# Kernel optimization log

Measured on AMD Instinct MI355X. Metric: run time of the kernel, lower is better.

The kernel has to match this reference:

```python
import jax, jax.numpy as jnp
import numpy as np

N_NODES = 50000
N_EDGES = 800000
IN_DIM = 100
HID = 128
OUT = 128
EPS = 1e-5


def setup_inputs() -> dict:
    key = jax.random.key(0)
    ks = jax.random.split(key, 12)
    x = jax.random.normal(ks[0], (N_NODES, IN_DIM), dtype=jnp.float32)
    edge_index = jax.random.randint(ks[1], (2, N_EDGES), 0, N_NODES, dtype=jnp.int32)
    def lin(k, i, o):
        return jax.random.normal(k, (i, o), dtype=jnp.float32) * (1.0 / np.sqrt(i))
    return {
        "x": x,
        "edge_index": edge_index,
        "W_l0": lin(ks[2], IN_DIM, HID),  # neighbor transform, layer 0
        "b_l0": jnp.zeros((HID,), jnp.float32),
        "W_r0": lin(ks[3], IN_DIM, HID),  # root transform, layer 0
        "gamma0": jnp.ones((HID,), jnp.float32),
        "beta0": jnp.zeros((HID,), jnp.float32),
        "W_l1": lin(ks[4], HID, OUT),
        "b_l1": jnp.zeros((OUT,), jnp.float32),
        "W_r1": lin(ks[5], HID, OUT),
        "gamma1": jnp.ones((OUT,), jnp.float32),
        "beta1": jnp.zeros((OUT,), jnp.float32),
    }


def _sage_conv(x, edge_index, W_l, b_l, W_r):
    # PyG SAGEConv (mean aggr): out = lin_l(mean_{j->i} x_j) + lin_r(x_i)
    src, dst = edge_index[0], edge_index[1]
    n = x.shape[0]
    msg_sum = jax.ops.segment_sum(x[src], dst, num_segments=n)        # [N, d_in]
    cnt = jax.ops.segment_sum(jnp.ones((src.shape[0],), x.dtype), dst, num_segments=n)
    agg = msg_sum / jnp.maximum(cnt, 1.0)[:, None]
    return agg @ W_l + b_l + x @ W_r


def _batch_norm(x, gamma, beta):
    # BatchNorm1d with batch statistics (training-mode math, biased var)
    mean = x.mean(axis=0)
    var = x.var(axis=0)
    return gamma * (x - mean) / jnp.sqrt(var + EPS) + beta


def reference(x, edge_index, W_l0, b_l0, W_r0, gamma0, beta0, W_l1, b_l1, W_r1, gamma1, beta1):
    # Layer 0: SAGEConv -> BN -> ReLU (dropout off for determinism)
    h = _sage_conv(x, edge_index, W_l0, b_l0, W_r0)
    h = jax.nn.relu(_batch_norm(h, gamma0, beta0))
    # Layer 1 (last): SAGEConv -> BN
    h = _sage_conv(h, edge_index, W_l1, b_l1, W_r1)
    return _batch_norm(h, gamma1, beta1)
```

## Files before the change

### kernel.cpp

```cpp
#include <hip/hip_runtime.h>
#include <hip/hip_bf16.h>

#define N_NODES 50000
#define N_EDGES 800000
#define NPAD    50048
#define IN_DIM  100
#define HID     128
#define BN_EPS  1e-5f

#define BSHIFT  6
#define BUCKS   782
#define BSTRIDE 2048
#define BCAP    2048
#define NSLICE  16

typedef unsigned int uint;
typedef unsigned short u16;
typedef __attribute__((ext_vector_type(8))) unsigned short us8;
typedef __attribute__((ext_vector_type(8))) short s8;
typedef __attribute__((ext_vector_type(4))) float f4;

__device__ __forceinline__ u16 f2bf(float f) {
    uint u = __builtin_bit_cast(uint, f);
    uint r = (u + 0x7FFFu + ((u >> 16) & 1u)) >> 16;
    return (u16)r;
}
__device__ __forceinline__ uint pack2(float a, float b) {
    return (uint)f2bf(a) | ((uint)f2bf(b) << 16);
}
__device__ __forceinline__ float bflo(uint p) { return __builtin_bit_cast(float, p << 16); }
__device__ __forceinline__ float bfhi(uint p) { return __builtin_bit_cast(float, p & 0xFFFF0000u); }

__global__ void init_cursor(int* __restrict__ bcursor) {
    int b = blockIdx.x * 256 + threadIdx.x;
    if (b < BUCKS) bcursor[b] = b * BSTRIDE;
}

__global__ __launch_bounds__(1024) void bucket_scatter_blk(
    const int* __restrict__ src, const int* __restrict__ dst,
    int* __restrict__ bcursor, uint* __restrict__ ebuf) {
    __shared__ int h[BUCKS];
    __shared__ int gb[BUCKS];
    int t = threadIdx.x;
    for (int i = t; i < BUCKS; i += 1024) h[i] = 0;
    __syncthreads();
    int base = blockIdx.x * 8192;
    int myb[8]; uint myv[8];
    #pragma unroll
    for (int r = 0; r < 8; ++r) {
        int e = base + r * 1024 + t;
        int b = -1; uint val = 0;
        if (e < N_EDGES) {
            int d = dst[e];
            b = d >> BSHIFT;
            val = (uint)src[e] | ((uint)(d & 63) << 16);
            atomicAdd(&h[b], 1);
        }
        myb[r] = b; myv[r] = val;
    }
    __syncthreads();
    for (int i = t; i < BUCKS; i += 1024) {
        int c = h[i];
        gb[i] = c ? atomicAdd(&bcursor[i], c) : 0;
        h[i] = 0;
    }
    __syncthreads();
    #pragma unroll
    for (int r = 0; r < 8; ++r) {
        int b = myb[r];
        if (b >= 0) {
            int pos = gb[b] + atomicAdd(&h[b], 1);
            ebuf[pos] = myv[r];
        }
    }
}

__global__ void cast_x_kernel(const float* __restrict__ x, u16* __restrict__ xb) {
    int idx = blockIdx.x * blockDim.x + threadIdx.x;
    if (idx >= NPAD * 128) return;
    int row = idx >> 7, k = idx & 127;
    float v = (row < N_NODES && k < IN_DIM) ? x[row * IN_DIM + k] : 0.f;
    xb[idx] = f2bf(v);
}

__global__ void cast_w_kernel(const float* __restrict__ W_l0, const float* __restrict__ W_r0,
                              const float* __restrict__ W_l1, const float* __restrict__ W_r1,
                              u16* __restrict__ d) {
    int w = blockIdx.y;
    const float* s = (w == 0) ? W_l0 : (w == 1) ? W_r0 : (w == 2) ? W_l1 : W_r1;
    int Ks = (w < 2) ? IN_DIM : HID;
    int idx = blockIdx.x * 256 + threadIdx.x;
    int n = idx >> 7, k = idx & 127;
    float v = (k < Ks) ? s[k * 128 + n] : 0.f;
    d[w * 16384 + idx] = f2bf(v);
}

__global__ __launch_bounds__(512) void agg_gemm(
    const uint* __restrict__ ebuf, const int* __restrict__ bcursor,
    const u16* __restrict__ X,
    const u16* __restrict__ WtL, const u16* __restrict__ WtR,
    const float* __restrict__ bias, float* __restrict__ out,
    float* __restrict__ gstats) {
    __shared__ u16 Aagg[64][136];
    __shared__ uint eL[BCAP];
    __shared__ u16 srcL[BCAP];
    __shared__ int cnt[64], ro[65], cur[64];
    __shared__ float s1L[128], s2L[128];

    int b = blockIdx.x;
    int t = threadIdx.x;
    int row0 = b * 64;
    int wave = t >> 6, lane = t & 63;
    int quad = lane >> 4, sub = lane & 15, l16 = lane & 15;

    int n = bcursor[b] - b * BSTRIDE;
    if (n > BCAP) n = BCAP;
    if (t < 64) cnt[t] = 0;
    if (t < 128) { s1L[t] = 0.f; s2L[t] = 0.f; }
    __syncthreads();
    for (int i = t; i < n; i += 512) {
        uint p = ebuf[b * BSTRIDE + i];
        eL[i] = p;
        atomicAdd(&cnt[p >> 16], 1);
    }
    __syncthreads();
    if (t < 64) {
        int v = cnt[t];
        int s = v;
        #pragma unroll
        for (int off = 1; off < 64; off <<= 1) {
            int u = __shfl_up(s, off, 64);
            if (t >= off) s += u;
        }
        ro[t] = s - v;
        cur[t] = s - v;
        if (t == 63) ro[64] = s;
    }
    __syncthreads();
    for (int i = t; i < n; i += 512) {
        uint p = eL[i];
        int pos = atomicAdd(&cur[p >> 16], 1);
        srcL[pos] = (u16)(p & 0xFFFFu);
    }
    __syncthreads();

    #pragma unroll
    for (int ni = 0; ni < 8; ++ni) {
        int nl = wave * 8 + ni;
        int node = row0 + nl;
        if (node >= N_NODES) {
            if (quad == 0) {
                uint4 z = make_uint4(0, 0, 0, 0);
                *(uint4*)&Aagg[nl][sub * 8] = z;
            }
            continue;
        }
        int rb = ro[nl], re = ro[nl + 1];
        float a0 = 0.f, a1 = 0.f, a2 = 0.f, a3 = 0.f;
        float a4 = 0.f, a5 = 0.f, a6 = 0.f, a7 = 0.f;
        int e = rb;
        for (; e + 16 <= re; e += 16) {
            int s0 = srcL[e + quad];
            int s1 = srcL[e + 4 + quad];
            int s2 = srcL[e + 8 + quad];
            int s3 = srcL[e + 12 + quad];
            uint4 v0 = ((const uint4*)(X + (size_t)s0 * 128))[sub];
            uint4 v1 = ((const uint4*)(X + (size_t)s1 * 128))[sub];
            uint4 v2 = ((const uint4*)(X + (size_t)s2 * 128))[sub];
            uint4 v3 = ((const uint4*)(X + (size_t)s3 * 128))[sub];
            a0 += (bflo(v0.x) + bflo(v1.x)) + (bflo(v2.x) + bflo(v3.x));
            a1 += (bfhi(v0.x) + bfhi(v1.x)) + (bfhi(v2.x) + bfhi(v3.x));
            a2 += (bflo(v0.y) + bflo(v1.y)) + (bflo(v2.y) + bflo(v3.y));
            a3 += (bfhi(v0.y) + bfhi(v1.y)) + (bfhi(v2.y) + bfhi(v3.y));
            a4 += (bflo(v0.z) + bflo(v1.z)) + (bflo(v2.z) + bflo(v3.z));
            a5 += (bfhi(v0.z) + bfhi(v1.z)) + (bfhi(v2.z) + bfhi(v3.z));
            a6 += (bflo(v0.w) + bflo(v1.w)) + (bflo(v2.w) + bflo(v3.w));
            a7 += (bfhi(v0.w) + bfhi(v1.w)) + (bfhi(v2.w) + bfhi(v3.w));
        }
        for (; e + 8 <= re; e += 8) {
            int s0 = srcL[e + quad];
            int s1 = srcL[e + 4 + quad];
            uint4 v0 = ((const uint4*)(X + (size_t)s0 * 128))[sub];
            uint4 v1 = ((const uint4*)(X + (size_t)s1 * 128))[sub];
            a0 += bflo(v0.x) + bflo(v1.x);
            a1 += bfhi(v0.x) + bfhi(v1.x);
            a2 += bflo(v0.y) + bflo(v1.y);
            a3 += bfhi(v0.y) + bfhi(v1.y);
            a4 += bflo(v0.z) + bflo(v1.z);
            a5 += bfhi(v0.z) + bfhi(v1.z);
            a6 += bflo(v0.w) + bflo(v1.w);
            a7 += bfhi(v0.w) + bfhi(v1.w);
        }
        for (; e < re; e += 4) {
            int ee = e + quad;
            if (ee < re) {
                int s0 = srcL[ee];
                uint4 v0 = ((const uint4*)(X + (size_t)s0 * 128))[sub];
                a0 += bflo(v0.x); a1 += bfhi(v0.x);
                a2 += bflo(v0.y); a3 += bfhi(v0.y);
                a4 += bflo(v0.z); a5 += bfhi(v0.z);
                a6 += bflo(v0.w); a7 += bfhi(v0.w);
            }
        }
        #pragma unroll
        for (int m = 16; m <= 32; m <<= 1) {
            a0 += __shfl_xor(a0, m, 64); a1 += __shfl_xor(a1, m, 64);
            a2 += __shfl_xor(a2, m, 64); a3 += __shfl_xor(a3, m, 64);
            a4 += __shfl_xor(a4, m, 64); a5 += __shfl_xor(a5, m, 64);
            a6 += __shfl_xor(a6, m, 64); a7 += __shfl_xor(a7, m, 64);
        }
        if (quad == 0) {
            float inv = 1.0f / fmaxf((float)(re - rb), 1.0f);
            uint4 o;
            o.x = pack2(a0 * inv, a1 * inv);
            o.y = pack2(a2 * inv, a3 * inv);
            o.z = pack2(a4 * inv, a5 * inv);
            o.w = pack2(a6 * inv, a7 * inv);
            *(uint4*)&Aagg[nl][sub * 8] = o;
        }
    }
    __syncthreads();

    int rm = (wave & 3) * 16;
    int cn = (wave >> 2) * 64;
    f4 acc[4];
    #pragma unroll
    for (int j = 0; j < 4; j++) acc[j] = (f4)0.f;

    #pragma unroll
    for (int k0 = 0; k0 < 128; k0 += 32) {
        s8 af = *(const s8*)&Aagg[rm + l16][k0 + quad * 8];
        #pragma unroll
        for (int nt = 0; nt < 4; ++nt) {
            s8 bfr = *(const s8*)(WtL + (cn + nt * 16 + l16) * 128 + k0 + quad * 8);
            acc[nt] = __builtin_amdgcn_mfma_f32_16x16x32_bf16(af, bfr, acc[nt], 0, 0, 0);
        }
    }
    #pragma unroll
    for (int k0 = 0; k0 < 128; k0 += 32) {
        s8 af = *(const s8*)(X + (size_t)(row0 + rm + l16) * 128 + k0 + quad * 8);
        #pragma unroll
        for (int nt = 0; nt < 4; ++nt) {
            s8 bfr = *(const s8*)(WtR + (cn + nt * 16 + l16) * 128 + k0 + quad * 8);
            acc[nt] = __builtin_amdgcn_mfma_f32_16x16x32_bf16(af, bfr, acc[nt], 0, 0, 0);
        }
    }

    #pragma unroll
    for (int nt = 0; nt < 4; ++nt) {
        int col = cn + nt * 16 + l16;
        float bv = bias[col];
        float s1 = 0.f, s2 = 0.f;
        #pragma unroll
        for (int r = 0; r < 4; ++r) {
            int row = row0 + rm + quad * 4 + r;
            if (row < N_NODES) {
                float v = acc[nt][r] + bv;
                out[(size_t)row * 128 + col] = v;
                s1 += v;
                s2 = fmaf(v, v, s2);
            }
        }
        s1 += __shfl_xor(s1, 16, 64); s2 += __shfl_xor(s2, 16, 64);
        s1 += __shfl_xor(s1, 32, 64); s2 += __shfl_xor(s2, 32, 64);
        if (quad == 0) {
            atomicAdd(&s1L[col], s1);
            atomicAdd(&s2L[col], s2);
        }
    }
    __syncthreads();
    int slice = b & (NSLICE - 1);
    if (t < 128) {
        atomicAdd(&gstats[slice * 256 + t], s1L[t]);
        atomicAdd(&gstats[slice * 256 + 128 + t], s2L[t]);
    }
}

__global__ void bn_relu_cast_kernel(const float* __restrict__ h,
                                    const float* __restrict__ gstats,
                                    const float* __restrict__ gamma,
                                    const float* __restrict__ beta,
                                    u16* __restrict__ hb, float inv_n, int total4) {
    __shared__ float ss[256];
    int t = threadIdx.x;
    if (t < 128) {
        float m = 0.f, q = 0.f;
        #pragma unroll
        for (int s = 0; s < NSLICE; ++s) {
            m += gstats[s * 256 + t];
            q += gstats[s * 256 + 128 + t];
        }
        float mean = m * inv_n;
        float var = q * inv_n - mean * mean;
        float inv = 1.0f / sqrtf(var + BN_EPS);
        float sc = gamma[t] * inv;
        ss[t] = sc;
        ss[128 + t] = beta[t] - mean * sc;
    }
    __syncthreads();
    int gid = blockIdx.x * 256 + t;
    if (gid < 768) {
        ((uint4*)(hb + (size_t)N_NODES * 128))[gid] = make_uint4(0, 0, 0, 0);
    }
    for (int i = gid; i < total4; i += gridDim.x * 256) {
        int cg = i & 31;
        float4 v = ((const float4*)h)[i];
        float4 sc = *(const float4*)&ss[cg * 4];
        float4 sh = *(const float4*)&ss[128 + cg * 4];
        float r0 = fmaxf(fmaf(v.x, sc.x, sh.x), 0.f);
        float r1 = fmaxf(fmaf(v.y, sc.y, sh.y), 0.f);
        float r2 = fmaxf(fmaf(v.z, sc.z, sh.z), 0.f);
        float r3 = fmaxf(fmaf(v.w, sc.w, sh.w), 0.f);
        uint2 o;
        o.x = pack2(r0, r1);
        o.y = pack2(r2, r3);
        ((uint2*)hb)[i] = o;
    }
}

__global__ void bn_apply_kernel(float* __restrict__ h,
                                const float* __restrict__ gstats,
                                const float* __restrict__ gamma,
                                const float* __restrict__ beta,
                                float inv_n, int total4) {
    __shared__ float ss[256];
    int t = threadIdx.x;
    if (t < 128) {
        float m = 0.f, q = 0.f;
        #pragma unroll
        for (int s = 0; s < NSLICE; ++s) {
            m += gstats[s * 256 + t];
            q += gstats[s * 256 + 128 + t];
        }
        float mean = m * inv_n;
        float var = q * inv_n - mean * mean;
        float inv = 1.0f / sqrtf(var + BN_EPS);
        float sc = gamma[t] * inv;
        ss[t] = sc;
        ss[128 + t] = beta[t] - mean * sc;
    }
    __syncthreads();
    for (int i = blockIdx.x * 256 + t; i < total4; i += gridDim.x * 256) {
        int cg = i & 31;
        float4 v = ((float4*)h)[i];
        float4 sc = *(const float4*)&ss[cg * 4];
        float4 sh = *(const float4*)&ss[128 + cg * 4];
        v.x = fmaf(v.x, sc.x, sh.x);
        v.y = fmaf(v.y, sc.y, sh.y);
        v.z = fmaf(v.z, sc.z, sh.z);
        v.w = fmaf(v.w, sc.w, sh.w);
        ((float4*)h)[i] = v;
    }
}

extern "C" void kernel_launch(void* const* d_in, const int* in_sizes, int n_in,
                              void* d_out, int out_size, void* d_ws, size_t ws_size,
                              hipStream_t stream) {
    const float* x      = (const float*)d_in[0];
    const int*   ei     = (const int*)d_in[1];
    const float* W_l0   = (const float*)d_in[2];
    const float* b_l0   = (const float*)d_in[3];
    const float* W_r0   = (const float*)d_in[4];
    const float* gamma0 = (const float*)d_in[5];
    const float* beta0  = (const float*)d_in[6];
    const float* W_l1   = (const float*)d_in[7];
    const float* b_l1   = (const float*)d_in[8];
    const float* W_r1   = (const float*)d_in[9];
    const float* gamma1 = (const float*)d_in[10];
    const float* beta1  = (const float*)d_in[11];

    const int* src = ei;
    const int* dst = ei + N_EDGES;

    char* w = (char*)d_ws;
    auto alloc = [&](size_t bytes) {
        void* p = (void*)w;
        w += (bytes + 255) & ~(size_t)255;
        return p;
    };
    char* zbase    = w;
    float* gstats0 = (float*)alloc(sizeof(float) * NSLICE * 256);
    float* gstats1 = (float*)alloc(sizeof(float) * NSLICE * 256);
    size_t zbytes  = (size_t)(w - zbase);

    int* bcursor   = (int*)alloc(sizeof(int) * BUCKS);
    uint* ebuf     = (uint*)alloc(sizeof(uint) * BUCKS * BSTRIDE);
    u16* xb        = (u16*)alloc(sizeof(u16) * (size_t)NPAD * 128);
    u16* hb        = (u16*)alloc(sizeof(u16) * (size_t)NPAD * 128);
    u16* Wt        = (u16*)alloc(sizeof(u16) * 4 * 16384);
    float* outp    = (float*)d_out;

    hipMemsetAsync(zbase, 0, zbytes, stream);

    const float inv_n = 1.0f / (float)N_NODES;
    const int total4 = N_NODES * HID / 4;

    init_cursor<<<(BUCKS + 255) / 256, 256, 0, stream>>>(bcursor);
    bucket_scatter_blk<<<(N_EDGES + 8191) / 8192, 1024, 0, stream>>>(src, dst, bcursor, ebuf);
    cast_x_kernel<<<(NPAD * 128 + 255) / 256, 256, 0, stream>>>(x, xb);
    cast_w_kernel<<<dim3(64, 4), 256, 0, stream>>>(W_l0, W_r0, W_l1, W_r1, Wt);

    agg_gemm<<<BUCKS, 512, 0, stream>>>(ebuf, bcursor, xb, Wt, Wt + 16384, b_l0, outp, gstats0);
    bn_relu_cast_kernel<<<2048, 256, 0, stream>>>(outp, gstats0, gamma0, beta0, hb, inv_n, total4);

    agg_gemm<<<BUCKS, 512, 0, stream>>>(ebuf, bcursor, hb, Wt + 2 * 16384, Wt + 3 * 16384, b_l1, outp, gstats1);
    bn_apply_kernel<<<2048, 256, 0, stream>>>(outp, gstats1, gamma1, beta1, inv_n, total4);
}
```

Baseline: 253.5 us.

## Emit layer-0 output as bf16, normalize in place, and use 32x32 MFMA tiles

The first aggregation+GEMM kernel now writes its pre-BN activations directly as bf16 into the hidden buffer instead of fp32. A new in-place BN+ReLU kernel then rewrites that bf16 buffer 8 values at a time, removing the fp32 write and read round trip of the layer-0 activations. The GEMM epilogue also switches from 16x16x32 to 32x32x16 bf16 MFMA tiles with register prefetch of the next k-slice. BN statistics are still accumulated in fp32, but normalization is applied to bf16-rounded values, which adds a little rounding error. The padding rows of the hidden buffer are no longer zeroed, though they only feed output rows that are masked off.

```diff
diff --git a/kernel.cpp b/kernel.cpp
--- a/kernel.cpp
+++ b/kernel.cpp
@@ -18,7 +18,7 @@
 typedef unsigned short u16;
 typedef __attribute__((ext_vector_type(8))) unsigned short us8;
 typedef __attribute__((ext_vector_type(8))) short s8;
-typedef __attribute__((ext_vector_type(4))) float f4;
+typedef __attribute__((ext_vector_type(16))) float f16v;
 
 __device__ __forceinline__ u16 f2bf(float f) {
     uint u = __builtin_bit_cast(uint, f);
@@ -95,11 +95,13 @@
     d[w * 16384 + idx] = f2bf(v);
 }
 
+template <int WRITE_BF16>
 __global__ __launch_bounds__(512) void agg_gemm(
     const uint* __restrict__ ebuf, const int* __restrict__ bcursor,
     const u16* __restrict__ X,
     const u16* __restrict__ WtL, const u16* __restrict__ WtR,
-    const float* __restrict__ bias, float* __restrict__ out,
+    const float* __restrict__ bias,
+    float* __restrict__ outf, u16* __restrict__ outb,
     float* __restrict__ gstats) {
     __shared__ u16 Aagg[64][136];
     __shared__ uint eL[BCAP];
@@ -111,7 +113,7 @@
     int t = threadIdx.x;
     int row0 = b * 64;
     int wave = t >> 6, lane = t & 63;
-    int quad = lane >> 4, sub = lane & 15, l16 = lane & 15;
+    int quad = lane >> 4, sub = lane & 15;
 
     int n = bcursor[b] - b * BSTRIDE;
     if (n > BCAP) n = BCAP;
@@ -149,10 +151,7 @@
         int nl = wave * 8 + ni;
         int node = row0 + nl;
         if (node >= N_NODES) {
-            if (quad == 0) {
-                uint4 z = make_uint4(0, 0, 0, 0);
-                *(uint4*)&Aagg[nl][sub * 8] = z;
-            }
+            if (quad == 0) *(uint4*)&Aagg[nl][sub * 8] = make_uint4(0, 0, 0, 0);
             continue;
         }
         int rb = ro[nl], re = ro[nl + 1];
@@ -221,49 +220,61 @@
     }
     __syncthreads();
 
-    int rm = (wave & 3) * 16;
-    int cn = (wave >> 2) * 64;
-    f4 acc[4];
-    #pragma unroll
-    for (int j = 0; j < 4; j++) acc[j] = (f4)0.f;
-
-    #pragma unroll
-    for (int k0 = 0; k0 < 128; k0 += 32) {
-        s8 af = *(const s8*)&Aagg[rm + l16][k0 + quad * 8];
-        #pragma unroll
-        for (int nt = 0; nt < 4; ++nt) {
-            s8 bfr = *(const s8*)(WtL + (cn + nt * 16 + l16) * 128 + k0 + quad * 8);
-            acc[nt] = __builtin_amdgcn_mfma_f32_16x16x32_bf16(af, bfr, acc[nt], 0, 0, 0);
-        }
-    }
-    #pragma unroll
-    for (int k0 = 0; k0 < 128; k0 += 32) {
-        s8 af = *(const s8*)(X + (size_t)(row0 + rm + l16) * 128 + k0 + quad * 8);
-        #pragma unroll
-        for (int nt = 0; nt < 4; ++nt) {
-            s8 bfr = *(const s8*)(WtR + (cn + nt * 16 + l16) * 128 + k0 + quad * 8);
-            acc[nt] = __builtin_amdgcn_mfma_f32_16x16x32_bf16(af, bfr, acc[nt], 0, 0, 0);
-        }
-    }
-
-    #pragma unroll
-    for (int nt = 0; nt < 4; ++nt) {
-        int col = cn + nt * 16 + l16;
+    int m31 = lane & 31;
+    int kh  = lane >> 5;
+    int rm = (wave & 1) * 32;
+    int cn = (wave >> 1) * 32;
+    f16v acc = (f16v)0.f;
+
+    {
+        s8 a_nxt = *(const s8*)&Aagg[rm + m31][kh * 8];
+        s8 b_nxt = *(const s8*)(WtL + (cn + m31) * 128 + kh * 8);
+        #pragma unroll
+        for (int ks = 0; ks < 8; ++ks) {
+            s8 a_cur = a_nxt, b_cur = b_nxt;
+            if (ks < 7) {
+                a_nxt = *(const s8*)&Aagg[rm + m31][(ks + 1) * 16 + kh * 8];
+                b_nxt = *(const s8*)(WtL + (cn + m31) * 128 + (ks + 1) * 16 + kh * 8);
+            }
+            acc = __builtin_amdgcn_mfma_f32_32x32x16_bf16(a_cur, b_cur, acc, 0, 0, 0);
+        }
+    }
+    {
+        const u16* xrow = X + (size_t)(row0 + rm + m31) * 128;
+        s8 a_nxt = *(const s8*)(xrow + kh * 8);
+        s8 b_nxt = *(const s8*)(WtR + (cn + m31) * 128 + kh * 8);
+        #pragma unroll
+        for (int ks = 0; ks < 8; ++ks) {
+            s8 a_cur = a_nxt, b_cur = b_nxt;
+            if (ks < 7) {
+                a_nxt = *(const s8*)(xrow + (ks + 1) * 16 + kh * 8);
+                b_nxt = *(const s8*)(WtR + (cn + m31) * 128 + (ks + 1) * 16 + kh * 8);
+            }
+            acc = __builtin_amdgcn_mfma_f32_32x32x16_bf16(a_cur, b_cur, acc, 0, 0, 0);
+        }
+    }
+
+    {
+        int col = cn + m31;
         float bv = bias[col];
         float s1 = 0.f, s2 = 0.f;
         #pragma unroll
-        for (int r = 0; r < 4; ++r) {
-            int row = row0 + rm + quad * 4 + r;
+        for (int reg = 0; reg < 16; ++reg) {
+            int rowin = (reg & 3) + 8 * (reg >> 2) + 4 * kh;
+            int row = row0 + rm + rowin;
             if (row < N_NODES) {
-                float v = acc[nt][r] + bv;
-                out[(size_t)row * 128 + col] = v;
+                float v = acc[reg] + bv;
+                if (WRITE_BF16)
+                    outb[(size_t)row * 128 + col] = f2bf(v);
+                else
+                    outf[(size_t)row * 128 + col] = v;
                 s1 += v;
                 s2 = fmaf(v, v, s2);
             }
         }
-        s1 += __shfl_xor(s1, 16, 64); s2 += __shfl_xor(s2, 16, 64);
-        s1 += __shfl_xor(s1, 32, 64); s2 += __shfl_xor(s2, 32, 64);
-        if (quad == 0) {
+        s1 += __shfl_xor(s1, 32, 64);
+        s2 += __shfl_xor(s2, 32, 64);
+        if (lane < 32) {
             atomicAdd(&s1L[col], s1);
             atomicAdd(&s2L[col], s2);
         }
@@ -276,11 +287,11 @@
     }
 }
 
-__global__ void bn_relu_cast_kernel(const float* __restrict__ h,
-                                    const float* __restrict__ gstats,
-                                    const float* __restrict__ gamma,
-                                    const float* __restrict__ beta,
-                                    u16* __restrict__ hb, float inv_n, int total4) {
+__global__ void bn_relu_inplace(u16* __restrict__ hb,
+                                const float* __restrict__ gstats,
+                                const float* __restrict__ gamma,
+                                const float* __restrict__ beta,
+                                float inv_n, int totalv) {
     __shared__ float ss[256];
     int t = threadIdx.x;
     if (t < 128) {
@@ -298,23 +309,27 @@
         ss[128 + t] = beta[t] - mean * sc;
     }
     __syncthreads();
-    int gid = blockIdx.x * 256 + t;
-    if (gid < 768) {
-        ((uint4*)(hb + (size_t)N_NODES * 128))[gid] = make_uint4(0, 0, 0, 0);
-    }
-    for (int i = gid; i < total4; i += gridDim.x * 256) {
-        int cg = i & 31;
-        float4 v = ((const float4*)h)[i];
-        float4 sc = *(const float4*)&ss[cg * 4];
-        float4 sh = *(const float4*)&ss[128 + cg * 4];
-        float r0 = fmaxf(fmaf(v.x, sc.x, sh.x), 0.f);
-        float r1 = fmaxf(fmaf(v.y, sc.y, sh.y), 0.f);
-        float r2 = fmaxf(fmaf(v.z, sc.z, sh.z), 0.f);
-        float r3 = fmaxf(fmaf(v.w, sc.w, sh.w), 0.f);
-        uint2 o;
+    for (int i = blockIdx.x * 256 + t; i < totalv; i += gridDim.x * 256) {
+        int cg = (i & 15) * 8;
+        uint4 p = ((const uint4*)hb)[i];
+        float4 scA = *(const float4*)&ss[cg];
+        float4 scB = *(const float4*)&ss[cg + 4];
+        float4 shA = *(const float4*)&ss[128 + cg];
+        float4 shB = *(const float4*)&ss[128 + cg + 4];
+        float r0 = fmaxf(fmaf(bflo(p.x), scA.x, shA.x), 0.f);
+        float r1 = fmaxf(fmaf(bfhi(p.x), scA.y, shA.y), 0.f);
+        float r2 = fmaxf(fmaf(bflo(p.y), scA.z, shA.z), 0.f);
+        float r3 = fmaxf(fmaf(bfhi(p.y), scA.w, shA.w), 0.f);
+        float r4 = fmaxf(fmaf(bflo(p.z), scB.x, shB.x), 0.f);
+        float r5 = fmaxf(fmaf(bfhi(p.z), scB.y, shB.y), 0.f);
+        float r6 = fmaxf(fmaf(bflo(p.w), scB.z, shB.z), 0.f);
+        float r7 = fmaxf(fmaf(bfhi(p.w), scB.w, shB.w), 0.f);
+        uint4 o;
         o.x = pack2(r0, r1);
         o.y = pack2(r2, r3);
-        ((uint2*)hb)[i] = o;
+        o.z = pack2(r4, r5);
+        o.w = pack2(r6, r7);
+        ((uint4*)hb)[i] = o;
     }
 }
 
@@ -394,15 +409,18 @@
 
     const float inv_n = 1.0f / (float)N_NODES;
     const int total4 = N_NODES * HID / 4;
+    const int totalv = N_NODES * HID / 8;
 
     init_cursor<<<(BUCKS + 255) / 256, 256, 0, stream>>>(bcursor);
     bucket_scatter_blk<<<(N_EDGES + 8191) / 8192, 1024, 0, stream>>>(src, dst, bcursor, ebuf);
     cast_x_kernel<<<(NPAD * 128 + 255) / 256, 256, 0, stream>>>(x, xb);
     cast_w_kernel<<<dim3(64, 4), 256, 0, stream>>>(W_l0, W_r0, W_l1, W_r1, Wt);
 
-    agg_gemm<<<BUCKS, 512, 0, stream>>>(ebuf, bcursor, xb, Wt, Wt + 16384, b_l0, outp, gstats0);
-    bn_relu_cast_kernel<<<2048, 256, 0, stream>>>(outp, gstats0, gamma0, beta0, hb, inv_n, total4);
-
-    agg_gemm<<<BUCKS, 512, 0, stream>>>(ebuf, bcursor, hb, Wt + 2 * 16384, Wt + 3 * 16384, b_l1, outp, gstats1);
+    agg_gemm<1><<<BUCKS, 512, 0, stream>>>(ebuf, bcursor, xb, Wt, Wt + 16384, b_l0,
+                                           nullptr, hb, gstats0);
+    bn_relu_inplace<<<1024, 256, 0, stream>>>(hb, gstats0, gamma0, beta0, inv_n, totalv);
+
+    agg_gemm<0><<<BUCKS, 512, 0, stream>>>(ebuf, bcursor, hb, Wt + 2 * 16384, Wt + 3 * 16384,
+                                           b_l1, outp, nullptr, gstats1);
     bn_apply_kernel<<<2048, 256, 0, stream>>>(outp, gstats1, gamma1, beta1, inv_n, total4);
 }
```

New measurement: 232.9 us. 1.09x faster.
